# Optimization experiments

Measured on AMD Instinct MI355X. Metric: run time of the kernel, lower is better.

Reference implementation:

```python
import jax, jax.numpy as jnp
import numpy as np

M, K, L, D_OUT = 8, 12, 9, 32           # ferns, bits/fern, patch size, vote dim
N, C, H, W = 64, 8, 128, 128            # batch, channels, image size
HP, WP = H - L + 1, W - L + 1           # valid word-map size (120, 120)
POOL = 7                                # AvgPool2d kernel, stride 1
TEMP = 0.1                              # soft-bit annealing temperature


def setup_inputs() -> dict:
    key = jax.random.key(0)
    ks = jax.random.split(key, 5)
    x = jax.random.normal(ks[0], (N, C, H, W), dtype=jnp.float32)
    thresholds = jax.random.normal(ks[1], (M, K), dtype=jnp.float32) * 0.1
    table = jax.random.normal(ks[2], (M, 2 ** K, D_OUT), dtype=jnp.float32) * 0.05
    chan_idx = jax.random.randint(ks[3], (M, K, 2), 0, C, dtype=jnp.int32)
    offsets = jax.random.randint(ks[4], (M, K, 2, 2), 0, L, dtype=jnp.int32)
    return dict(x=x, thresholds=thresholds, table=table,
                chan_idx=chan_idx, offsets=offsets)


def _shifted_plane(x, c, dy, dx):
    # x: (N,C,H,W) -> (N,HP,WP) pixel plane at channel c shifted by (dy,dx)
    return jax.lax.dynamic_slice(x, (0, c, dy, dx), (N, 1, HP, WP))[:, 0]


def reference(x, thresholds, table, chan_idx, offsets):
    # --- FernBitWord: K thresholded pixel-pair differences per fern ---
    def bit_fn(c2, off2):
        p1 = _shifted_plane(x, c2[0], off2[0, 0], off2[0, 1])
        p2 = _shifted_plane(x, c2[1], off2[1, 0], off2[1, 1])
        return p1 - p2                                   # (N,HP,WP)

    flat_c = chan_idx.reshape(M * K, 2)
    flat_o = offsets.reshape(M * K, 2, 2)
    diff = jax.vmap(bit_fn)(flat_c, flat_o).reshape(M, K, N, HP, WP)

    s = jax.nn.sigmoid((diff - thresholds[:, :, None, None, None]) / TEMP)
    bits = s > 0.5                                       # hard bit values
    pow2 = (2 ** jnp.arange(K, dtype=jnp.int32))[None, :, None, None, None]
    words = jnp.sum(bits.astype(jnp.int32) * pow2, axis=1)   # (M,N,HP,WP)
    conf = jnp.prod(jnp.where(bits, s, 1.0 - s), axis=1)     # (M,N,HP,WP)

    # --- FernSparseTable: per-fern voting-table lookup, accumulated over ferns ---
    def step(acc, mkw):
        tbl_m, w_m, c_m = mkw
        return acc + tbl_m[w_m] * c_m[..., None], None   # (N,HP,WP,D)

    init = jnp.zeros((N, HP, WP, D_OUT), dtype=x.dtype)
    votes, _ = jax.lax.scan(step, init, (table, words, conf))
    votes = jnp.transpose(votes, (0, 3, 1, 2))           # (N,D,HP,WP)

    # --- AvgPool2d(kernel=POOL, stride=1) + flatten ---
    pooled = jax.lax.reduce_window(
        votes, 0.0, jax.lax.add, (1, 1, POOL, POOL), (1, 1, 1, 1), 'VALID'
    ) / (POOL * POOL)
    return pooled.reshape(N, -1)
```

## Files before the change

kernel.cpp:

```cpp
#include <hip/hip_runtime.h>
#include <hip/hip_fp16.h>


#define NN 64
#define CC 8
#define HH 128
#define WW 128
#define MM 8
#define KK 12
#define DD 32
#define OUTS 114
#define TT 19
#define PT 25
#define XT 33
#define XSTRIDE (XT*XT)
#define VSTRIDE 36
#define NPOSI (PT*PT)
#define THREADS 640
#define POOLW 7

#define PTK 24
#define XTK 32
#define NPOS_IMG (120*120)
#define K1_THREADS (PTK*PTK)

#define VOTE_BYTES ((size_t)NN * NPOS_IMG * DD * 2)

#define LDS_BYTES (CC*XSTRIDE*4 + NPOSI*VSTRIDE*2)

__device__ __forceinline__ float4 ld4h(const __half* p) {
    union { float2 f; __half2 h[2]; } u;
    u.f = *(const float2*)p;
    float2 a = __half22float2(u.h[0]);
    float2 b = __half22float2(u.h[1]);
    return make_float4(a.x, a.y, b.x, b.y);
}
__device__ __forceinline__ void st4h(__half* p, float4 v) {
    union { float2 f; __half2 h[2]; } u;
    u.h[0] = __floats2half2_rn(v.x, v.y);
    u.h[1] = __floats2half2_rn(v.z, v.w);
    *(float2*)p = u.f;
}

template<int XS, int XROW>
__device__ __forceinline__ void fern_bits(const float* __restrict__ xs, int pb,
                                          const float* __restrict__ thresholds,
                                          const int*   __restrict__ chan_idx,
                                          const int*   __restrict__ offsets,
                                          unsigned wreg[MM], float creg[MM])
{
    #pragma unroll
    for (int m = 0; m < MM; ++m) {
        unsigned word = 0u;
        float P = 1.f;
        #pragma unroll
        for (int k = 0; k < KK; ++k) {
            const int mk = m*KK + k;
            int c1  = chan_idx[mk*2 + 0];
            int c2  = chan_idx[mk*2 + 1];
            int dy1 = offsets[mk*4 + 0];
            int dx1 = offsets[mk*4 + 1];
            int dy2 = offsets[mk*4 + 2];
            int dx2 = offsets[mk*4 + 3];
            float thr = thresholds[mk];
            float p1 = xs[c1*XS + dy1*XROW + dx1 + pb];
            float p2 = xs[c2*XS + dy2*XROW + dx2 + pb];
            float z  = (p1 - p2) - thr;
            if (z > 0.f) word |= (1u << k);
            float e = __expf(-10.f * fabsf(z));
            P += P * e;
        }
        wreg[m] = word;
        creg[m] = __builtin_amdgcn_rcpf(P);
    }
}

__global__ __launch_bounds__(K1_THREADS, 8)
void fern_gather(const float* __restrict__ x,
                 const float* __restrict__ thresholds,
                 const float* __restrict__ table,
                 const int*   __restrict__ chan_idx,
                 const int*   __restrict__ offsets,
                 __half* __restrict__ votes)
{
    __shared__ float4 xs4[CC*XTK*XTK/4];
    float* xs = (float*)xs4;

    const int tile = blockIdx.x;
    const int n    = tile / 25;
    const int t2   = tile - n*25;
    const int pi0  = (t2 / 5) * PTK;
    const int pj0  = (t2 % 5) * PTK;

    const int tid = threadIdx.x;

    const float* xn = x + (size_t)n * (CC*HH*WW);
    for (int idx = tid; idx < CC*XTK*XTK/4; idx += K1_THREADS) {
        int c   = idx >> 8;
        int rem = idx & 255;
        int r   = rem >> 3;
        int c4  = rem & 7;
        xs4[idx] = *(const float4*)(xn + (c*HH + pi0 + r)*WW + pj0 + c4*4);
    }
    __syncthreads();

    const int ty = tid / PTK;
    const int tx = tid - ty*PTK;

    unsigned wreg[MM];
    float    creg[MM];
    fern_bits<XTK*XTK, XTK>(xs, ty*XTK + tx, thresholds, chan_idx, offsets,
                            wreg, creg);
    __syncthreads();

    float4* cbuf = (float4*)xs;
    uint4*  wbuf = (uint4*)(xs + 4608);

    {
        uint4 wv;
        wv.x = wreg[0] | (wreg[1] << 16);
        wv.y = wreg[2] | (wreg[3] << 16);
        wv.z = wreg[4] | (wreg[5] << 16);
        wv.w = wreg[6] | (wreg[7] << 16);
        wbuf[tid] = wv;
        cbuf[tid*2 + 0] = make_float4(creg[0], creg[1], creg[2], creg[3]);
        cbuf[tid*2 + 1] = make_float4(creg[4], creg[5], creg[6], creg[7]);
    }
    __syncthreads();

    #pragma unroll
    for (int it = 0; it < 8; ++it) {
        const int item = tid + it*K1_THREADS;
        const int pos  = item >> 3;
        const int d4   = item & 7;
        uint4  wv = wbuf[pos];
        float4 c0 = cbuf[pos*2 + 0];
        float4 c1 = cbuf[pos*2 + 1];
        const float* tb = table + d4*4;
        float4 acc = make_float4(0.f, 0.f, 0.f, 0.f);
        unsigned w; float cf; float4 tv;
#define FERN(mi, wexpr, cexpr)                                             \
        w = (wexpr); cf = (cexpr);                                         \
        tv = *(const float4*)(tb + ((size_t)(mi) << 17) + w*DD);           \
        acc.x += cf*tv.x; acc.y += cf*tv.y;                                \
        acc.z += cf*tv.z; acc.w += cf*tv.w;
        FERN(0, wv.x & 0xFFFFu, c0.x)
        FERN(1, wv.x >> 16,     c0.y)
        FERN(2, wv.y & 0xFFFFu, c0.z)
        FERN(3, wv.y >> 16,     c0.w)
        FERN(4, wv.z & 0xFFFFu, c1.x)
        FERN(5, wv.z >> 16,     c1.y)
        FERN(6, wv.w & 0xFFFFu, c1.z)
        FERN(7, wv.w >> 16,     c1.w)
#undef FERN
        const int py = pos / PTK;
        const int px = pos - py*PTK;
        const int gp = n*NPOS_IMG + (pi0 + py)*120 + (pj0 + px);
        union { float2 f; __half2 h[2]; } u;
        u.h[0] = __floats2half2_rn(acc.x, acc.y);
        u.h[1] = __floats2half2_rn(acc.z, acc.w);
        *(float2*)(votes + (size_t)gp*DD + d4*4) = u.f;
    }
}

__global__ __launch_bounds__(THREADS, 8)
void fern_pool(const __half* __restrict__ votes,
               float* __restrict__ out)
{
    __shared__ float2 vsraw[NPOSI*VSTRIDE/4];
    __half* vs = (__half*)vsraw;

    const int tile = blockIdx.x;
    const int n    = tile / 36;
    const int t2   = tile - n*36;
    const int ti   = t2 / 6;
    const int tj   = t2 - ti*6;
    const int i0   = ti * TT;
    const int j0   = tj * TT;

    const int tid = threadIdx.x;

    const int pbase = n*NPOS_IMG + i0*120 + j0;
    for (int idx = tid; idx < NPOSI*8; idx += THREADS) {
        const int pos = idx >> 3;
        const int oct = idx & 7;
        const int y   = pos / PT;
        const int j   = pos - y*PT;
        const __half* src = votes + (size_t)(pbase + y*120 + j)*DD + oct*4;
        *(float2*)(vs + pos*VSTRIDE + oct*4) = *(const float2*)src;
    }
    __syncthreads();

    for (int w = tid; w < PT*8; w += THREADS) {
        int y  = w / 8;
        int d4 = w - y*8;
        float4 s = make_float4(0.f, 0.f, 0.f, 0.f);
        float4 ring[POOLW];
        #pragma unroll
        for (int j = 0; j < PT; ++j) {
            float4 v = ld4h(vs + (y*PT + j)*VSTRIDE + d4*4);
            if (j >= POOLW) {
                float4 o = ring[j % POOLW];
                s.x -= o.x; s.y -= o.y; s.z -= o.z; s.w -= o.w;
            }
            ring[j % POOLW] = v;
            s.x += v.x; s.y += v.y; s.z += v.z; s.w += v.w;
            if (j >= POOLW-1)
                st4h(vs + (y*PT + (j - POOLW + 1))*VSTRIDE + d4*4, s);
        }
    }
    __syncthreads();

    const float inv = 1.f / 49.f;
    float* outn = out + (size_t)n * (DD*OUTS*OUTS);
    for (int w = tid; w < 8*TT; w += THREADS) {
        int d4 = w / TT;
        int jo = w - d4*TT;
        float4 s = make_float4(0.f, 0.f, 0.f, 0.f);
        float4 ring[POOLW];
        #pragma unroll
        for (int y = 0; y < PT; ++y) {
            float4 v = ld4h(vs + (y*PT + jo)*VSTRIDE + d4*4);
            if (y >= POOLW) {
                float4 o = ring[y % POOLW];
                s.x -= o.x; s.y -= o.y; s.z -= o.z; s.w -= o.w;
            }
            ring[y % POOLW] = v;
            s.x += v.x; s.y += v.y; s.z += v.z; s.w += v.w;
            if (y >= POOLW-1) {
                int io = y - POOLW + 1;
                size_t base = ((size_t)(d4*4)*OUTS + (i0 + io))*OUTS + (j0 + jo);
                outn[base                      ] = s.x * inv;
                outn[base +   (size_t)OUTS*OUTS] = s.y * inv;
                outn[base + 2*(size_t)OUTS*OUTS] = s.z * inv;
                outn[base + 3*(size_t)OUTS*OUTS] = s.w * inv;
            }
        }
    }
}

__global__ __launch_bounds__(THREADS, 5)
void fern_fused(const float* __restrict__ x,
                const float* __restrict__ thresholds,
                const float* __restrict__ table,
                const int*   __restrict__ chan_idx,
                const int*   __restrict__ offsets,
                float* __restrict__ out)
{
    extern __shared__ float smem[];
    float*  xs = smem;
    __half* vs = (__half*)(smem + CC*XSTRIDE);

    const int tile = blockIdx.x;
    const int n    = tile / 36;
    const int t2   = tile - n*36;
    const int ti   = t2 / 6;
    const int tj   = t2 - ti*6;
    const int i0   = ti * TT;
    const int j0   = tj * TT;
    const int tid = threadIdx.x;

    const float* xn = x + (size_t)n * (CC*HH*WW);
    for (int idx = tid; idx < CC*XSTRIDE; idx += THREADS) {
        int c   = idx / XSTRIDE;
        int rem = idx - c*XSTRIDE;
        int r   = rem / XT;
        int col = rem - r*XT;
        xs[idx] = xn[(c*HH + (i0 + r))*WW + (j0 + col)];
    }
    __syncthreads();

    unsigned wreg[MM];
    float    creg[MM];
    if (tid < NPOSI) {
        const int y  = tid / PT;
        const int j  = tid - y*PT;
        fern_bits<XSTRIDE, XT>(xs, y*XT + j, thresholds, chan_idx, offsets,
                               wreg, creg);
    }
    __syncthreads();

    float* cbuf = smem;
    uint4* wbuf = (uint4*)(smem + 5000);

    if (tid < NPOSI) {
        uint4 wv;
        wv.x = wreg[0] | (wreg[1] << 16);
        wv.y = wreg[2] | (wreg[3] << 16);
        wv.z = wreg[4] | (wreg[5] << 16);
        wv.w = wreg[6] | (wreg[7] << 16);
        wbuf[tid] = wv;
        ((float4*)cbuf)[tid*2 + 0] = make_float4(creg[0], creg[1], creg[2], creg[3]);
        ((float4*)cbuf)[tid*2 + 1] = make_float4(creg[4], creg[5], creg[6], creg[7]);
    }
    __syncthreads();

    for (int item = tid; item < NPOSI*8; item += THREADS) {
        const int pos = item >> 3;
        const int d4  = item & 7;
        uint4  wv = wbuf[pos];
        float4 c0 = ((const float4*)cbuf)[pos*2 + 0];
        float4 c1 = ((const float4*)cbuf)[pos*2 + 1];
        const float* tb = table + d4*4;
        float4 acc = make_float4(0.f, 0.f, 0.f, 0.f);
        unsigned w; float cf; float4 tv;
#define FERN(mi, wexpr, cexpr)                                             \
        w = (wexpr); cf = (cexpr);                                         \
        tv = *(const float4*)(tb + ((size_t)(mi) << 17) + w*DD);           \
        acc.x += cf*tv.x; acc.y += cf*tv.y;                                \
        acc.z += cf*tv.z; acc.w += cf*tv.w;
        FERN(0, wv.x & 0xFFFFu, c0.x)
        FERN(1, wv.x >> 16,     c0.y)
        FERN(2, wv.y & 0xFFFFu, c0.z)
        FERN(3, wv.y >> 16,     c0.w)
        FERN(4, wv.z & 0xFFFFu, c1.x)
        FERN(5, wv.z >> 16,     c1.y)
        FERN(6, wv.w & 0xFFFFu, c1.z)
        FERN(7, wv.w >> 16,     c1.w)
#undef FERN
        st4h(vs + pos*VSTRIDE + d4*4, acc);
    }
    __syncthreads();

    for (int w = tid; w < PT*8; w += THREADS) {
        int y  = w / 8;
        int d4 = w - y*8;
        float4 s = make_float4(0.f, 0.f, 0.f, 0.f);
        float4 ring[POOLW];
        #pragma unroll
        for (int j = 0; j < PT; ++j) {
            float4 v = ld4h(vs + (y*PT + j)*VSTRIDE + d4*4);
            if (j >= POOLW) {
                float4 o = ring[j % POOLW];
                s.x -= o.x; s.y -= o.y; s.z -= o.z; s.w -= o.w;
            }
            ring[j % POOLW] = v;
            s.x += v.x; s.y += v.y; s.z += v.z; s.w += v.w;
            if (j >= POOLW-1)
                st4h(vs + (y*PT + (j - POOLW + 1))*VSTRIDE + d4*4, s);
        }
    }
    __syncthreads();

    const float inv = 1.f / 49.f;
    float* outn = out + (size_t)n * (DD*OUTS*OUTS);
    for (int w = tid; w < 8*TT; w += THREADS) {
        int d4 = w / TT;
        int jo = w - d4*TT;
        float4 s = make_float4(0.f, 0.f, 0.f, 0.f);
        float4 ring[POOLW];
        #pragma unroll
        for (int y = 0; y < PT; ++y) {
            float4 v = ld4h(vs + (y*PT + jo)*VSTRIDE + d4*4);
            if (y >= POOLW) {
                float4 o = ring[y % POOLW];
                s.x -= o.x; s.y -= o.y; s.z -= o.z; s.w -= o.w;
            }
            ring[y % POOLW] = v;
            s.x += v.x; s.y += v.y; s.z += v.z; s.w += v.w;
            if (y >= POOLW-1) {
                int io = y - POOLW + 1;
                size_t base = ((size_t)(d4*4)*OUTS + (i0 + io))*OUTS + (j0 + jo);
                outn[base                      ] = s.x * inv;
                outn[base +   (size_t)OUTS*OUTS] = s.y * inv;
                outn[base + 2*(size_t)OUTS*OUTS] = s.z * inv;
                outn[base + 3*(size_t)OUTS*OUTS] = s.w * inv;
            }
        }
    }
}

extern "C" void kernel_launch(void* const* d_in, const int* in_sizes, int n_in,
                              void* d_out, int out_size, void* d_ws, size_t ws_size,
                              hipStream_t stream) {
    const float* x          = (const float*)d_in[0];
    const float* thresholds = (const float*)d_in[1];
    const float* table      = (const float*)d_in[2];
    const int*   chan_idx   = (const int*)d_in[3];
    const int*   offsets    = (const int*)d_in[4];
    float* out = (float*)d_out;

    if (d_ws != nullptr && ws_size >= VOTE_BYTES) {
        __half* votes = (__half*)d_ws;
        fern_gather<<<dim3(NN*25), dim3(K1_THREADS), 0, stream>>>(
            x, thresholds, table, chan_idx, offsets, votes);
        fern_pool<<<dim3(NN*36), dim3(THREADS), 0, stream>>>(votes, out);
    } else {
        hipFuncSetAttribute((const void*)fern_fused,
                            hipFuncAttributeMaxDynamicSharedMemorySize, LDS_BYTES);
        fern_fused<<<dim3(NN*36), dim3(THREADS), LDS_BYTES, stream>>>(
            x, thresholds, table, chan_idx, offsets, out);
    }
}
```

Before: 335.1 us.

## Convert voting table to fp16 and gather 8 outputs per thread

Adds a pre-pass that converts the fp32 voting table to fp16 in workspace. The gather kernel then reads 16-byte fp16 rows covering 8 output dims per thread, halving table traffic and the number of gather loads, and stores 16-byte vote chunks. The coefficient buffer is split into two arrays and occupancy is lowered to 7 blocks. The cost is an extra kernel launch per call, fp16 rounding of the table weights, and a larger workspace requirement; if the workspace is too small, execution falls back to the fused path.

```diff
diff --git a/kernel.cpp b/kernel.cpp
--- a/kernel.cpp
+++ b/kernel.cpp
@@ -25,6 +25,8 @@
 #define K1_THREADS (PTK*PTK)
 
 #define VOTE_BYTES ((size_t)NN * NPOS_IMG * DD * 2)
+#define TAB_ELEMS  (MM*4096*DD)
+#define TAB16_BYTES ((size_t)TAB_ELEMS * 2)
 
 #define LDS_BYTES (CC*XSTRIDE*4 + NPOSI*VSTRIDE*2)
 
@@ -75,10 +77,24 @@
     }
 }
 
-__global__ __launch_bounds__(K1_THREADS, 8)
+__global__ __launch_bounds__(256)
+void table_to_f16(const float* __restrict__ t, __half* __restrict__ t16)
+{
+    const int i = (blockIdx.x * 256 + threadIdx.x) * 8;
+    float4 a = *(const float4*)(t + i);
+    float4 b = *(const float4*)(t + i + 4);
+    union { float4 f; __half2 h[4]; } o;
+    o.h[0] = __floats2half2_rn(a.x, a.y);
+    o.h[1] = __floats2half2_rn(a.z, a.w);
+    o.h[2] = __floats2half2_rn(b.x, b.y);
+    o.h[3] = __floats2half2_rn(b.z, b.w);
+    *(float4*)(t16 + i) = o.f;
+}
+
+__global__ __launch_bounds__(K1_THREADS, 7)
 void fern_gather(const float* __restrict__ x,
                  const float* __restrict__ thresholds,
-                 const float* __restrict__ table,
+                 const __half* __restrict__ table16,
                  const int*   __restrict__ chan_idx,
                  const int*   __restrict__ offsets,
                  __half* __restrict__ votes)
@@ -113,8 +129,9 @@
                             wreg, creg);
     __syncthreads();
 
-    float4* cbuf = (float4*)xs;
-    uint4*  wbuf = (uint4*)(xs + 4608);
+    float4* c0buf = (float4*)xs;
+    float4* c1buf = (float4*)(xs + 2304);
+    uint4*  wbuf  = (uint4*)(xs + 4608);
 
     {
         uint4 wv;
@@ -122,44 +139,54 @@
         wv.y = wreg[2] | (wreg[3] << 16);
         wv.z = wreg[4] | (wreg[5] << 16);
         wv.w = wreg[6] | (wreg[7] << 16);
-        wbuf[tid] = wv;
-        cbuf[tid*2 + 0] = make_float4(creg[0], creg[1], creg[2], creg[3]);
-        cbuf[tid*2 + 1] = make_float4(creg[4], creg[5], creg[6], creg[7]);
+        wbuf[tid]  = wv;
+        c0buf[tid] = make_float4(creg[0], creg[1], creg[2], creg[3]);
+        c1buf[tid] = make_float4(creg[4], creg[5], creg[6], creg[7]);
     }
     __syncthreads();
 
     #pragma unroll
-    for (int it = 0; it < 8; ++it) {
+    for (int it = 0; it < 4; ++it) {
         const int item = tid + it*K1_THREADS;
-        const int pos  = item >> 3;
-        const int d4   = item & 7;
+        const int pos  = item >> 2;
+        const int q    = item & 3;
         uint4  wv = wbuf[pos];
-        float4 c0 = cbuf[pos*2 + 0];
-        float4 c1 = cbuf[pos*2 + 1];
-        const float* tb = table + d4*4;
-        float4 acc = make_float4(0.f, 0.f, 0.f, 0.f);
-        unsigned w; float cf; float4 tv;
-#define FERN(mi, wexpr, cexpr)                                             \
-        w = (wexpr); cf = (cexpr);                                         \
-        tv = *(const float4*)(tb + ((size_t)(mi) << 17) + w*DD);           \
-        acc.x += cf*tv.x; acc.y += cf*tv.y;                                \
-        acc.z += cf*tv.z; acc.w += cf*tv.w;
-        FERN(0, wv.x & 0xFFFFu, c0.x)
-        FERN(1, wv.x >> 16,     c0.y)
-        FERN(2, wv.y & 0xFFFFu, c0.z)
-        FERN(3, wv.y >> 16,     c0.w)
-        FERN(4, wv.z & 0xFFFFu, c1.x)
-        FERN(5, wv.z >> 16,     c1.y)
-        FERN(6, wv.w & 0xFFFFu, c1.z)
-        FERN(7, wv.w >> 16,     c1.w)
-#undef FERN
+        float4 c0 = c0buf[pos];
+        float4 c1 = c1buf[pos];
+        const __half* tb = table16 + q*8;
+        float acc[8];
+        #pragma unroll
+        for (int j = 0; j < 8; ++j) acc[j] = 0.f;
+#define FERN16(mi, wexpr, cexpr) {                                         \
+        unsigned w = (wexpr); float cf = (cexpr);                          \
+        union { float4 f; __half2 h[4]; } u;                               \
+        u.f = *(const float4*)(tb + (((unsigned)(mi) << 12) + w)*DD);      \
+        float2 v0 = __half22float2(u.h[0]);                                \
+        float2 v1 = __half22float2(u.h[1]);                                \
+        float2 v2 = __half22float2(u.h[2]);                                \
+        float2 v3 = __half22float2(u.h[3]);                                \
+        acc[0] += cf*v0.x; acc[1] += cf*v0.y;                              \
+        acc[2] += cf*v1.x; acc[3] += cf*v1.y;                              \
+        acc[4] += cf*v2.x; acc[5] += cf*v2.y;                              \
+        acc[6] += cf*v3.x; acc[7] += cf*v3.y; }
+        FERN16(0, wv.x & 0xFFFFu, c0.x)
+        FERN16(1, wv.x >> 16,     c0.y)
+        FERN16(2, wv.y & 0xFFFFu, c0.z)
+        FERN16(3, wv.y >> 16,     c0.w)
+        FERN16(4, wv.z & 0xFFFFu, c1.x)
+        FERN16(5, wv.z >> 16,     c1.y)
+        FERN16(6, wv.w & 0xFFFFu, c1.z)
+        FERN16(7, wv.w >> 16,     c1.w)
+#undef FERN16
         const int py = pos / PTK;
         const int px = pos - py*PTK;
         const int gp = n*NPOS_IMG + (pi0 + py)*120 + (pj0 + px);
-        union { float2 f; __half2 h[2]; } u;
-        u.h[0] = __floats2half2_rn(acc.x, acc.y);
-        u.h[1] = __floats2half2_rn(acc.z, acc.w);
-        *(float2*)(votes + (size_t)gp*DD + d4*4) = u.f;
+        union { float4 f; __half2 h[4]; } o;
+        o.h[0] = __floats2half2_rn(acc[0], acc[1]);
+        o.h[1] = __floats2half2_rn(acc[2], acc[3]);
+        o.h[2] = __floats2half2_rn(acc[4], acc[5]);
+        o.h[3] = __floats2half2_rn(acc[6], acc[7]);
+        *(float4*)(votes + (size_t)gp*DD + q*8) = o.f;
     }
 }
 
@@ -380,10 +407,13 @@
     const int*   offsets    = (const int*)d_in[4];
     float* out = (float*)d_out;
 
-    if (d_ws != nullptr && ws_size >= VOTE_BYTES) {
+    if (d_ws != nullptr && ws_size >= VOTE_BYTES + TAB16_BYTES) {
         __half* votes = (__half*)d_ws;
+        __half* t16   = (__half*)((char*)d_ws + VOTE_BYTES);
+        table_to_f16<<<dim3(TAB_ELEMS/(256*8)), dim3(256), 0, stream>>>(
+            table, t16);
         fern_gather<<<dim3(NN*25), dim3(K1_THREADS), 0, stream>>>(
-            x, thresholds, table, chan_idx, offsets, votes);
+            x, thresholds, t16, chan_idx, offsets, votes);
         fern_pool<<<dim3(NN*36), dim3(THREADS), 0, stream>>>(votes, out);
     } else {
         hipFuncSetAttribute((const void*)fern_fused,
```

Result: faster. 321.0 us (-4.2%).
